# Kernel optimization log

Hardware: AMD Instinct MI355X
Metric: run time of the kernel (lower is better)

Reference implementation:

```python
import jax, jax.numpy as jnp
import numpy as np

N_NODES = 50000
N_EDGES = 800000
IN_CH, HID_CH, OUT_CH = 128, 128, 64


def setup_inputs() -> dict:
    key = jax.random.key(0)
    k1, k2, k3, k4, k5, k6 = jax.random.split(key, 6)
    x = jax.random.normal(k1, (N_NODES, IN_CH), dtype=jnp.float32)
    edge_index = jax.random.randint(k2, (2, N_EDGES), 0, N_NODES, dtype=jnp.int64)
    # nn.Linear params: W [out, in], b [out]
    W1 = jax.random.normal(k3, (HID_CH, IN_CH), dtype=jnp.float32) / np.sqrt(IN_CH)
    b1 = jax.random.normal(k4, (HID_CH,), dtype=jnp.float32) * 0.01
    W2 = jax.random.normal(k5, (OUT_CH, HID_CH), dtype=jnp.float32) / np.sqrt(HID_CH)
    b2 = jax.random.normal(k6, (OUT_CH,), dtype=jnp.float32) * 0.01
    return {"x": x, "edge_index": edge_index, "W1": W1, "b1": b1, "W2": W2, "b2": b2}


def _aggregate(x, edge_index):
    # Faithful to SimpleGNN.aggregate: deg from ROW counts, normalization gathered at DST (col).
    row, col = edge_index[0], edge_index[1]
    n = x.shape[0]
    deg = jnp.bincount(row, length=n).astype(x.dtype)
    deg_inv = jnp.where(deg > 0, 1.0 / deg, 0.0)
    # out[dst] += x[src] * deg_inv[dst]  ==  segment_sum(x[src] by dst) * deg_inv[dst]
    agg = jax.ops.segment_sum(x[row], col, num_segments=n)
    return agg * deg_inv[:, None]


def reference(x, edge_index, W1, b1, W2, b2):
    h = x @ W1.T + b1                 # [N, hidden]
    h = _aggregate(h, edge_index)     # degree-normalized scatter-add
    out = h @ W2.T + b2               # [N, out]
    return out
```

## Files before the change

kernel.cpp:

```cpp
#include <hip/hip_runtime.h>
#include <hip/hip_bf16.h>


#define IN_CH   128
#define OUT_CH  64
#define NCHUNK  64
#define NRANGE_H 4
#define RBINS_H 12544
#define MC_PAD  40
#define YROWS   32
#define PLACE_BLOCKS 256
#define SMEM_FLOATS (IN_CH * OUT_CH + YROWS * (IN_CH + 4))

typedef unsigned short u16;
typedef unsigned int u32;

static __device__ inline float bfu32_lo(u32 u) { return __uint_as_float(u << 16); }
static __device__ inline float bfu32_hi(u32 u) { return __uint_as_float(u & 0xffff0000u); }
static __device__ inline u16 f2bf(float f) {
    __hip_bfloat16 h = __float2bfloat16(f);
    return *reinterpret_cast<u16*>(&h);
}

static __device__ inline int detect_stride_wave(const int* __restrict__ ei) {
    int lane = threadIdx.x & 63;
    int idx = (lane < 32) ? (2 * lane + 1) : 1;
    int v = ei[idx];
    unsigned long long m = __ballot((v != 0) && (lane < 32));
    return (m == 0ull) ? 2 : 1;
}

static __device__ inline void y_unit(int t, const float* __restrict__ x,
                                     const float* __restrict__ M,
                                     u16* __restrict__ y, float* smem,
                                     int n_nodes) {
    int tid = threadIdx.x;
    float* Ms = smem;
    float (*xs)[IN_CH + 4] = (float(*)[IN_CH + 4])(smem + IN_CH * OUT_CH);
    int tx = tid & 15;
    int ty = tid >> 4;
    int row0 = t * YROWS;
    if (row0 >= n_nodes) return;

    const float4* Mv = (const float4*)M;
    float4* Msv = (float4*)Ms;
#pragma unroll
    for (int k = 0; k < 8; ++k) Msv[tid + 256 * k] = Mv[tid + 256 * k];

    for (int f = tid; f < YROWS * 32; f += 256) {
        int r = f >> 5, kq = f & 31;
        float4 v = make_float4(0.f, 0.f, 0.f, 0.f);
        if (row0 + r < n_nodes)
            v = *(const float4*)&x[(size_t)(row0 + r) * IN_CH + 4 * kq];
        *(float4*)&xs[r][4 * kq] = v;
    }
    __syncthreads();

    float4 acc0 = make_float4(0.f, 0.f, 0.f, 0.f);
    float4 acc1 = make_float4(0.f, 0.f, 0.f, 0.f);

    for (int k = 0; k < IN_CH; k += 4) {
        float4 xr0 = *(const float4*)&xs[ty][k];
        float4 xr1 = *(const float4*)&xs[ty + 16][k];
        float4 m0 = *(const float4*)&Ms[(k + 0) * OUT_CH + 4 * tx];
        float4 m1 = *(const float4*)&Ms[(k + 1) * OUT_CH + 4 * tx];
        float4 m2 = *(const float4*)&Ms[(k + 2) * OUT_CH + 4 * tx];
        float4 m3 = *(const float4*)&Ms[(k + 3) * OUT_CH + 4 * tx];
        acc0.x = fmaf(xr0.x, m0.x, acc0.x); acc0.y = fmaf(xr0.x, m0.y, acc0.y);
        acc0.z = fmaf(xr0.x, m0.z, acc0.z); acc0.w = fmaf(xr0.x, m0.w, acc0.w);
        acc0.x = fmaf(xr0.y, m1.x, acc0.x); acc0.y = fmaf(xr0.y, m1.y, acc0.y);
        acc0.z = fmaf(xr0.y, m1.z, acc0.z); acc0.w = fmaf(xr0.y, m1.w, acc0.w);
        acc0.x = fmaf(xr0.z, m2.x, acc0.x); acc0.y = fmaf(xr0.z, m2.y, acc0.y);
        acc0.z = fmaf(xr0.z, m2.z, acc0.z); acc0.w = fmaf(xr0.z, m2.w, acc0.w);
        acc0.x = fmaf(xr0.w, m3.x, acc0.x); acc0.y = fmaf(xr0.w, m3.y, acc0.y);
        acc0.z = fmaf(xr0.w, m3.z, acc0.z); acc0.w = fmaf(xr0.w, m3.w, acc0.w);
        acc1.x = fmaf(xr1.x, m0.x, acc1.x); acc1.y = fmaf(xr1.x, m0.y, acc1.y);
        acc1.z = fmaf(xr1.x, m0.z, acc1.z); acc1.w = fmaf(xr1.x, m0.w, acc1.w);
        acc1.x = fmaf(xr1.y, m1.x, acc1.x); acc1.y = fmaf(xr1.y, m1.y, acc1.y);
        acc1.z = fmaf(xr1.y, m1.z, acc1.z); acc1.w = fmaf(xr1.y, m1.w, acc1.w);
        acc1.x = fmaf(xr1.z, m2.x, acc1.x); acc1.y = fmaf(xr1.z, m2.y, acc1.y);
        acc1.z = fmaf(xr1.z, m2.z, acc1.z); acc1.w = fmaf(xr1.z, m2.w, acc1.w);
        acc1.x = fmaf(xr1.w, m3.x, acc1.x); acc1.y = fmaf(xr1.w, m3.y, acc1.y);
        acc1.z = fmaf(xr1.w, m3.z, acc1.z); acc1.w = fmaf(xr1.w, m3.w, acc1.w);
    }

    int r0 = row0 + ty;
    int r1 = row0 + ty + 16;
    if (r0 < n_nodes) {
        ushort4 s4;
        s4.x = f2bf(acc0.x); s4.y = f2bf(acc0.y);
        s4.z = f2bf(acc0.z); s4.w = f2bf(acc0.w);
        *(ushort4*)&y[(size_t)r0 * OUT_CH + 4 * tx] = s4;
    }
    if (r1 < n_nodes) {
        ushort4 s4;
        s4.x = f2bf(acc1.x); s4.y = f2bf(acc1.y);
        s4.z = f2bf(acc1.z); s4.w = f2bf(acc1.w);
        *(ushort4*)&y[(size_t)r1 * OUT_CH + 4 * tx] = s4;
    }
}

__global__ __launch_bounds__(256) void mk_prep(const float* __restrict__ W1,
                                               const float* __restrict__ b1,
                                               const float* __restrict__ W2,
                                               const int* __restrict__ ei,
                                               float* __restrict__ M,
                                               float* __restrict__ c,
                                               u16* __restrict__ row_slab,
                                               u16* __restrict__ col_slab,
                                               u16* __restrict__ erank,
                                               int* __restrict__ counter,
                                               int n_edges, int n_nodes) {
    __shared__ u32 bins[RBINS_H];
    int b = blockIdx.x;
    int tid = threadIdx.x;
    if (b < MC_PAD) {
        if (b == 0 && tid == 0) *counter = 0;
        int t = b * 256 + tid;
        if (t < IN_CH * OUT_CH) {
            int o = t & (OUT_CH - 1);
            int i = t >> 6;
            float acc = 0.f;
            for (int h = 0; h < 128; ++h)
                acc += W1[h * 128 + i] * W2[o * 128 + h];
            M[i * OUT_CH + o] = acc;
        } else if (t < IN_CH * OUT_CH + OUT_CH) {
            int o = t - IN_CH * OUT_CH;
            float acc = 0.f;
            for (int h = 0; h < 128; ++h)
                acc += b1[h] * W2[o * 128 + h];
            c[o] = acc;
        }
        return;
    }
    int hb = b - MC_PAD;
    int chunk = hb & (NCHUNK - 1);
    int range = hb >> 6;

    int range_size = (n_nodes + NRANGE_H - 1) / NRANGE_H;
    int lo = range * range_size;
    int hi = lo + range_size; if (hi > n_nodes) hi = n_nodes;
    int nbins = hi - lo;
    if (nbins <= 0) return;

    int stride = detect_stride_wave(ei);
    for (int i = tid; i < nbins; i += 256) bins[i] = 0u;
    __syncthreads();

    size_t e0 = (size_t)chunk * n_edges / NCHUNK;
    size_t e1 = (size_t)(chunk + 1) * n_edges / NCHUNK;
    size_t cnt = e1 - e0;
    const int* rp = ei;
    const int* cp = ei + (size_t)n_edges * stride;

    size_t i = tid;
    int s[8], d[8];
    for (; i + 1792 < cnt; i += 2048) {
#pragma unroll
        for (int k = 0; k < 8; ++k) s[k] = rp[(e0 + i + 256 * k) * stride];
#pragma unroll
        for (int k = 0; k < 8; ++k) d[k] = cp[(e0 + i + 256 * k) * stride];
#pragma unroll
        for (int k = 0; k < 8; ++k) {
            if (s[k] >= lo && s[k] < hi) atomicAdd(&bins[s[k] - lo], 1u);
            if (d[k] >= lo && d[k] < hi && (unsigned)s[k] < (unsigned)n_nodes) {
                u32 old = atomicAdd(&bins[d[k] - lo], 0x10000u);
                erank[e0 + i + 256 * k] = (u16)(old >> 16);
            }
        }
    }
    for (; i < cnt; i += 256) {
        int ss = rp[(e0 + i) * stride];
        int dd = cp[(e0 + i) * stride];
        if (ss >= lo && ss < hi) atomicAdd(&bins[ss - lo], 1u);
        if (dd >= lo && dd < hi && (unsigned)ss < (unsigned)n_nodes) {
            u32 old = atomicAdd(&bins[dd - lo], 0x10000u);
            erank[e0 + i] = (u16)(old >> 16);
        }
    }
    __syncthreads();

    size_t base = (size_t)chunk * n_nodes + lo;
    for (int k = tid; k < nbins; k += 256) {
        u32 v = bins[k];
        row_slab[base + k] = (u16)(v & 0xFFFFu);
        col_slab[base + k] = (u16)(v >> 16);
    }
}

__global__ __launch_bounds__(256) void mk_choff(u16* __restrict__ row_slab,
                                                u16* __restrict__ col_slab,
                                                int* __restrict__ deg_row,
                                                int* __restrict__ cnt_col,
                                                int* __restrict__ cursor_part,
                                                int* __restrict__ bsums,
                                                int* __restrict__ counter,
                                                int* __restrict__ bscan_g,
                                                int n_nodes, int nb) {
    __shared__ int sm[256];
    __shared__ int islast;
    int b = blockIdx.x;
    int t = threadIdx.x;
    int n = b * 256 + t;
    int run = 0;
    if (n < n_nodes) {
        int sum = 0;
#pragma unroll 8
        for (int ch = 0; ch < NCHUNK; ++ch)
            sum += row_slab[(size_t)ch * n_nodes + n];
        deg_row[n] = sum;
#pragma unroll 8
        for (int ch = 0; ch < NCHUNK; ++ch) {
            int v = col_slab[(size_t)ch * n_nodes + n];
            col_slab[(size_t)ch * n_nodes + n] = (u16)run;
            run += v;
        }
        cnt_col[n] = run;
    }
    sm[t] = run;
    __syncthreads();
    for (int d = 1; d < 256; d <<= 1) {
        int add = (t >= d) ? sm[t - d] : 0;
        __syncthreads();
        sm[t] += add;
        __syncthreads();
    }
    if (n < n_nodes) cursor_part[n] = sm[t] - run;
    if (t == 255) bsums[b] = sm[t];

    __syncthreads();
    if (t == 0) {
        __threadfence();
        int old = atomicAdd(counter, 1);
        islast = (old == nb - 1);
    }
    __syncthreads();
    if (islast) {
        int v = (t < nb) ? atomicAdd(&bsums[t], 0) : 0;
        sm[t] = v;
        __syncthreads();
        for (int d = 1; d < 256; d <<= 1) {
            int add = (t >= d) ? sm[t - d] : 0;
            __syncthreads();
            sm[t] += add;
            __syncthreads();
        }
        bscan_g[t] = sm[t] - v;
    }
}

__global__ __launch_bounds__(256) void mk_place_y(const int* __restrict__ ei,
                                                  const int* __restrict__ cursor_part,
                                                  const int* __restrict__ bscan_g,
                                                  const u16* __restrict__ col_slab,
                                                  const u16* __restrict__ erank,
                                                  int* __restrict__ csr_src,
                                                  const float* __restrict__ x,
                                                  const float* __restrict__ M,
                                                  u16* __restrict__ y,
                                                  int n_edges, int n_nodes) {
    __shared__ float smem[SMEM_FLOATS];
    int b = blockIdx.x;
    int tid = threadIdx.x;

    if (b < PLACE_BLOCKS) {
        int* bscanL = (int*)smem;
        bscanL[tid] = bscan_g[tid];
        __syncthreads();

        int chunk = b >> 2;
        int sub = b & 3;
        int stride = detect_stride_wave(ei);

        size_t e0 = (size_t)chunk * n_edges / NCHUNK;
        size_t e1 = (size_t)(chunk + 1) * n_edges / NCHUNK;
        size_t cnt = e1 - e0;
        size_t s0 = e0 + (size_t)sub * cnt / 4;
        size_t s1 = e0 + (size_t)(sub + 1) * cnt / 4;
        const int* rp = ei;
        const int* cp = ei + (size_t)n_edges * stride;
        size_t slab_base = (size_t)chunk * n_nodes;

        size_t i = s0 + tid;
        int s4[4], d4[4], cpart[4], coff[4];
        u16 r4[4];
        for (; i + 768 < s1; i += 1024) {
#pragma unroll
            for (int k = 0; k < 4; ++k) s4[k] = rp[(i + 256 * k) * stride];
#pragma unroll
            for (int k = 0; k < 4; ++k) d4[k] = cp[(i + 256 * k) * stride];
#pragma unroll
            for (int k = 0; k < 4; ++k) r4[k] = erank[i + 256 * k];
#pragma unroll
            for (int k = 0; k < 4; ++k) {
                int dc = ((unsigned)d4[k] < (unsigned)n_nodes) ? d4[k] : 0;
                cpart[k] = cursor_part[dc];
                coff[k]  = (int)col_slab[slab_base + dc];
            }
#pragma unroll
            for (int k = 0; k < 4; ++k) {
                if ((unsigned)d4[k] < (unsigned)n_nodes &&
                    (unsigned)s4[k] < (unsigned)n_nodes) {
                    csr_src[cpart[k] + bscanL[d4[k] >> 8] + coff[k] + (int)r4[k]] = s4[k];
                }
            }
        }
        for (; i < s1; i += 256) {
            int ss = rp[i * stride];
            int dd = cp[i * stride];
            if ((unsigned)dd < (unsigned)n_nodes && (unsigned)ss < (unsigned)n_nodes) {
                csr_src[cursor_part[dd] + bscanL[dd >> 8] +
                        (int)col_slab[slab_base + dd] + (int)erank[i]] = ss;
            }
        }
        return;
    }

    y_unit(b - PLACE_BLOCKS, x, M, y, smem, n_nodes);
}

__global__ __launch_bounds__(256) void mk_agg_final(const int* __restrict__ cursor_part,
                                                    const int* __restrict__ bscan_g,
                                                    const int* __restrict__ cnt_col,
                                                    const int* __restrict__ csr_src,
                                                    const int* __restrict__ deg_row,
                                                    const uint2* __restrict__ yv,
                                                    const float* __restrict__ c,
                                                    const float* __restrict__ b2,
                                                    float* __restrict__ out,
                                                    int n_nodes) {
    int wave = threadIdx.x >> 6;
    int lane = threadIdx.x & 63;
    int dsub = lane >> 4;
    int ch   = lane & 15;
    int d = blockIdx.x * 16 + wave * 4 + dsub;
    if (d >= n_nodes) return;

    int start = cursor_part[d] + bscan_g[d >> 8];
    int cnt = cnt_col[d];
    int end = start + cnt;
    int e1m = end - 1;
    float a0 = 0.f, a1 = 0.f, a2 = 0.f, a3 = 0.f;
    for (int j = start; j < end; j += 8) {
        int idx[8], srcs[8];
#pragma unroll
        for (int k = 0; k < 8; ++k) {
            int t = j + k;
            idx[k] = t > e1m ? e1m : t;
        }
#pragma unroll
        for (int k = 0; k < 8; ++k) srcs[k] = csr_src[idx[k]];
        uint2 u[8];
#pragma unroll
        for (int k = 0; k < 8; ++k) u[k] = yv[(size_t)srcs[k] * 16 + ch];
#pragma unroll
        for (int k = 1; k < 8; ++k)
            if (j + k >= end) { u[k].x = 0u; u[k].y = 0u; }
#pragma unroll
        for (int k = 0; k < 8; ++k) {
            a0 += bfu32_lo(u[k].x);
            a1 += bfu32_hi(u[k].x);
            a2 += bfu32_lo(u[k].y);
            a3 += bfu32_hi(u[k].y);
        }
    }
    int dr = deg_row[d];
    float di = (dr > 0) ? (1.0f / (float)dr) : 0.f;
    float fc = di * (float)cnt;
    float4 cv = ((const float4*)c)[ch];
    float4 bv = ((const float4*)b2)[ch];
    float4 o;
    o.x = di * a0 + fc * cv.x + bv.x;
    o.y = di * a1 + fc * cv.y + bv.y;
    o.z = di * a2 + fc * cv.z + bv.z;
    o.w = di * a3 + fc * cv.w + bv.w;
    ((float4*)(out + (size_t)d * OUT_CH))[ch] = o;
}

extern "C" void kernel_launch(void* const* d_in, const int* in_sizes, int n_in,
                              void* d_out, int out_size, void* d_ws, size_t ws_size,
                              hipStream_t stream) {
    const float* x  = (const float*)d_in[0];
    const int*   ei = (const int*)d_in[1];
    const float* W1 = (const float*)d_in[2];
    const float* b1 = (const float*)d_in[3];
    const float* W2 = (const float*)d_in[4];
    const float* b2 = (const float*)d_in[5];
    float* out = (float*)d_out;

    const int n_nodes = in_sizes[0] / IN_CH;
    const int n_edges = in_sizes[1] / 2;

    const size_t slab_bytes = (((size_t)NCHUNK * n_nodes * 2) + 127) & ~(size_t)127;
    const size_t csr_bytes  = ((size_t)n_edges * 4 + 127) & ~(size_t)127;
    const size_t y_bytes    = ((size_t)n_nodes * OUT_CH * 2 + 127) & ~(size_t)127;

    char* ws = (char*)d_ws;
    float* M        = (float*)(ws);
    float* c        = (float*)(ws + 32768);
    int*   deg_row  = (int*)  (ws + 33152);
    int*   cnt_col  = (int*)  (ws + 233216);
    int*   cursor   = (int*)  (ws + 433280);
    int*   bsums    = (int*)  (ws + 633344);
    int*   bscan_g  = (int*)  (ws + 634368);
    int*   counter  = (int*)  (ws + 635392);
    u16*   row_slab = (u16*)  (ws + 635520);
    u16*   col_slab = (u16*)  (ws + 635520 + slab_bytes);
    int*   csr_src  = (int*)  (ws + 635520 + 2 * slab_bytes);
    u16*   y        = (u16*)  (ws + 635520 + 2 * slab_bytes + csr_bytes);
    u16*   erank    = (u16*)  (ws + 635520 + 2 * slab_bytes + csr_bytes + y_bytes);

    const int y_total = (n_nodes + YROWS - 1) / YROWS;
    const int nb = (n_nodes + 255) / 256;

    mk_prep<<<MC_PAD + NCHUNK * NRANGE_H, 256, 0, stream>>>(
        W1, b1, W2, ei, M, c, row_slab, col_slab, erank, counter,
        n_edges, n_nodes);

    mk_choff<<<nb, 256, 0, stream>>>(row_slab, col_slab, deg_row, cnt_col,
                                     cursor, bsums, counter, bscan_g,
                                     n_nodes, nb);

    mk_place_y<<<PLACE_BLOCKS + y_total, 256, 0, stream>>>(
        ei, cursor, bscan_g, col_slab, erank, csr_src, x, M, y,
        n_edges, n_nodes);

    mk_agg_final<<<(n_nodes + 15) / 16, 256, 0, stream>>>(
        cursor, bscan_g, cnt_col, csr_src, deg_row, (const uint2*)y, c, b2, out,
        n_nodes);
}
```

Before: 158.4 us.

## Replace chunked shared-memory histogram slabs with global atomics for CSR build

Drops the per-chunk LDS histograms, u16 slab arrays and per-edge rank array used to build the destination-sorted CSR. Degree and column counts now come from global atomicAdd directly, and placement uses atomic cursor increments on the exclusive scan. This removes the slab write/read traffic and the 64-chunk reduction pass, and adds a zeroing kernel. The cost is heavy global atomic contention and a nondeterministic edge order within each destination. The aggregation start offset is recomputed from the post-increment cursor.

New measurement: 222.2 us. 40.3% more time.

```diff
diff --git a/kernel.cpp b/kernel.cpp
--- a/kernel.cpp
+++ b/kernel.cpp
@@ -4,12 +4,9 @@
 
 #define IN_CH   128
 #define OUT_CH  64
-#define NCHUNK  64
-#define NRANGE_H 4
-#define RBINS_H 12544
-#define MC_PAD  40
+#define MC_UNITS 33
 #define YROWS   32
-#define PLACE_BLOCKS 256
+#define EPB     2048
 #define SMEM_FLOATS (IN_CH * OUT_CH + YROWS * (IN_CH + 4))
 
 typedef unsigned short u16;
@@ -100,22 +97,25 @@
     }
 }
 
+__global__ __launch_bounds__(256) void mk_zero(float4* __restrict__ p, int n4,
+                                               int* __restrict__ counter) {
+    int i = blockIdx.x * 256 + threadIdx.x;
+    if (i < n4) p[i] = make_float4(0.f, 0.f, 0.f, 0.f);
+    if (i == 0) *counter = 0;
+}
+
 __global__ __launch_bounds__(256) void mk_prep(const float* __restrict__ W1,
                                                const float* __restrict__ b1,
                                                const float* __restrict__ W2,
                                                const int* __restrict__ ei,
                                                float* __restrict__ M,
                                                float* __restrict__ c,
-                                               u16* __restrict__ row_slab,
-                                               u16* __restrict__ col_slab,
-                                               u16* __restrict__ erank,
-                                               int* __restrict__ counter,
+                                               int* __restrict__ deg_row,
+                                               int* __restrict__ cnt_col,
                                                int n_edges, int n_nodes) {
-    __shared__ u32 bins[RBINS_H];
     int b = blockIdx.x;
     int tid = threadIdx.x;
-    if (b < MC_PAD) {
-        if (b == 0 && tid == 0) *counter = 0;
+    if (b < MC_UNITS) {
         int t = b * 256 + tid;
         if (t < IN_CH * OUT_CH) {
             int o = t & (OUT_CH - 1);
@@ -133,90 +133,53 @@
         }
         return;
     }
-    int hb = b - MC_PAD;
-    int chunk = hb & (NCHUNK - 1);
-    int range = hb >> 6;
-
-    int range_size = (n_nodes + NRANGE_H - 1) / NRANGE_H;
-    int lo = range * range_size;
-    int hi = lo + range_size; if (hi > n_nodes) hi = n_nodes;
-    int nbins = hi - lo;
-    if (nbins <= 0) return;
-
+    int db = b - MC_UNITS;
+    size_t e0 = (size_t)db * EPB;
+    if (e0 >= (size_t)n_edges) return;
     int stride = detect_stride_wave(ei);
-    for (int i = tid; i < nbins; i += 256) bins[i] = 0u;
-    __syncthreads();
-
-    size_t e0 = (size_t)chunk * n_edges / NCHUNK;
-    size_t e1 = (size_t)(chunk + 1) * n_edges / NCHUNK;
-    size_t cnt = e1 - e0;
     const int* rp = ei;
     const int* cp = ei + (size_t)n_edges * stride;
 
-    size_t i = tid;
-    int s[8], d[8];
-    for (; i + 1792 < cnt; i += 2048) {
-#pragma unroll
-        for (int k = 0; k < 8; ++k) s[k] = rp[(e0 + i + 256 * k) * stride];
-#pragma unroll
-        for (int k = 0; k < 8; ++k) d[k] = cp[(e0 + i + 256 * k) * stride];
+    size_t i0 = e0 + (size_t)tid * 8;
+    if (i0 + 8 <= (size_t)n_edges) {
+        int s8[8], d8[8];
+#pragma unroll
+        for (int k = 0; k < 8; ++k) s8[k] = rp[(i0 + k) * stride];
+#pragma unroll
+        for (int k = 0; k < 8; ++k) d8[k] = cp[(i0 + k) * stride];
 #pragma unroll
         for (int k = 0; k < 8; ++k) {
-            if (s[k] >= lo && s[k] < hi) atomicAdd(&bins[s[k] - lo], 1u);
-            if (d[k] >= lo && d[k] < hi && (unsigned)s[k] < (unsigned)n_nodes) {
-                u32 old = atomicAdd(&bins[d[k] - lo], 0x10000u);
-                erank[e0 + i + 256 * k] = (u16)(old >> 16);
-            }
-        }
-    }
-    for (; i < cnt; i += 256) {
-        int ss = rp[(e0 + i) * stride];
-        int dd = cp[(e0 + i) * stride];
-        if (ss >= lo && ss < hi) atomicAdd(&bins[ss - lo], 1u);
-        if (dd >= lo && dd < hi && (unsigned)ss < (unsigned)n_nodes) {
-            u32 old = atomicAdd(&bins[dd - lo], 0x10000u);
-            erank[e0 + i] = (u16)(old >> 16);
-        }
-    }
-    __syncthreads();
-
-    size_t base = (size_t)chunk * n_nodes + lo;
-    for (int k = tid; k < nbins; k += 256) {
-        u32 v = bins[k];
-        row_slab[base + k] = (u16)(v & 0xFFFFu);
-        col_slab[base + k] = (u16)(v >> 16);
-    }
-}
-
-__global__ __launch_bounds__(256) void mk_choff(u16* __restrict__ row_slab,
-                                                u16* __restrict__ col_slab,
-                                                int* __restrict__ deg_row,
-                                                int* __restrict__ cnt_col,
-                                                int* __restrict__ cursor_part,
-                                                int* __restrict__ bsums,
-                                                int* __restrict__ counter,
-                                                int* __restrict__ bscan_g,
-                                                int n_nodes, int nb) {
+            if ((unsigned)s8[k] < (unsigned)n_nodes) {
+                atomicAdd(&deg_row[s8[k]], 1);
+                if ((unsigned)d8[k] < (unsigned)n_nodes)
+                    atomicAdd(&cnt_col[d8[k]], 1);
+            }
+        }
+    } else {
+        for (size_t i = i0; i < (size_t)n_edges && i < i0 + 8; ++i) {
+            int ss = rp[i * stride];
+            int dd = cp[i * stride];
+            if ((unsigned)ss < (unsigned)n_nodes) {
+                atomicAdd(&deg_row[ss], 1);
+                if ((unsigned)dd < (unsigned)n_nodes)
+                    atomicAdd(&cnt_col[dd], 1);
+            }
+        }
+    }
+}
+
+__global__ __launch_bounds__(256) void mk_scan(const int* __restrict__ cnt_col,
+                                               int* __restrict__ cursor_part,
+                                               int* __restrict__ bsums,
+                                               int* __restrict__ counter,
+                                               int* __restrict__ bscan_g,
+                                               int n_nodes, int nb) {
     __shared__ int sm[256];
     __shared__ int islast;
     int b = blockIdx.x;
     int t = threadIdx.x;
     int n = b * 256 + t;
-    int run = 0;
-    if (n < n_nodes) {
-        int sum = 0;
-#pragma unroll 8
-        for (int ch = 0; ch < NCHUNK; ++ch)
-            sum += row_slab[(size_t)ch * n_nodes + n];
-        deg_row[n] = sum;
-#pragma unroll 8
-        for (int ch = 0; ch < NCHUNK; ++ch) {
-            int v = col_slab[(size_t)ch * n_nodes + n];
-            col_slab[(size_t)ch * n_nodes + n] = (u16)run;
-            run += v;
-        }
-        cnt_col[n] = run;
-    }
+    int run = (n < n_nodes) ? cnt_col[n] : 0;
     sm[t] = run;
     __syncthreads();
     for (int d = 1; d < 256; d <<= 1) {
@@ -250,73 +213,62 @@
 }
 
 __global__ __launch_bounds__(256) void mk_place_y(const int* __restrict__ ei,
-                                                  const int* __restrict__ cursor_part,
+                                                  int* __restrict__ cursor_part,
                                                   const int* __restrict__ bscan_g,
-                                                  const u16* __restrict__ col_slab,
-                                                  const u16* __restrict__ erank,
                                                   int* __restrict__ csr_src,
                                                   const float* __restrict__ x,
                                                   const float* __restrict__ M,
                                                   u16* __restrict__ y,
-                                                  int n_edges, int n_nodes) {
+                                                  int n_edges, int n_nodes,
+                                                  int place_blocks) {
     __shared__ float smem[SMEM_FLOATS];
     int b = blockIdx.x;
     int tid = threadIdx.x;
 
-    if (b < PLACE_BLOCKS) {
+    if (b < place_blocks) {
         int* bscanL = (int*)smem;
         bscanL[tid] = bscan_g[tid];
         __syncthreads();
 
-        int chunk = b >> 2;
-        int sub = b & 3;
+        size_t e0 = (size_t)b * EPB;
+        if (e0 >= (size_t)n_edges) return;
         int stride = detect_stride_wave(ei);
-
-        size_t e0 = (size_t)chunk * n_edges / NCHUNK;
-        size_t e1 = (size_t)(chunk + 1) * n_edges / NCHUNK;
-        size_t cnt = e1 - e0;
-        size_t s0 = e0 + (size_t)sub * cnt / 4;
-        size_t s1 = e0 + (size_t)(sub + 1) * cnt / 4;
         const int* rp = ei;
         const int* cp = ei + (size_t)n_edges * stride;
-        size_t slab_base = (size_t)chunk * n_nodes;
-
-        size_t i = s0 + tid;
-        int s4[4], d4[4], cpart[4], coff[4];
-        u16 r4[4];
-        for (; i + 768 < s1; i += 1024) {
-#pragma unroll
-            for (int k = 0; k < 4; ++k) s4[k] = rp[(i + 256 * k) * stride];
-#pragma unroll
-            for (int k = 0; k < 4; ++k) d4[k] = cp[(i + 256 * k) * stride];
-#pragma unroll
-            for (int k = 0; k < 4; ++k) r4[k] = erank[i + 256 * k];
-#pragma unroll
-            for (int k = 0; k < 4; ++k) {
-                int dc = ((unsigned)d4[k] < (unsigned)n_nodes) ? d4[k] : 0;
-                cpart[k] = cursor_part[dc];
-                coff[k]  = (int)col_slab[slab_base + dc];
-            }
-#pragma unroll
-            for (int k = 0; k < 4; ++k) {
-                if ((unsigned)d4[k] < (unsigned)n_nodes &&
-                    (unsigned)s4[k] < (unsigned)n_nodes) {
-                    csr_src[cpart[k] + bscanL[d4[k] >> 8] + coff[k] + (int)r4[k]] = s4[k];
+
+        size_t i0 = e0 + (size_t)tid * 8;
+        if (i0 + 8 <= (size_t)n_edges) {
+            int s8[8], d8[8], pos[8];
+#pragma unroll
+            for (int k = 0; k < 8; ++k) s8[k] = rp[(i0 + k) * stride];
+#pragma unroll
+            for (int k = 0; k < 8; ++k) d8[k] = cp[(i0 + k) * stride];
+#pragma unroll
+            for (int k = 0; k < 8; ++k) {
+                bool v = (unsigned)d8[k] < (unsigned)n_nodes &&
+                         (unsigned)s8[k] < (unsigned)n_nodes;
+                pos[k] = v ? atomicAdd(&cursor_part[d8[k]], 1) : -1;
+            }
+#pragma unroll
+            for (int k = 0; k < 8; ++k) {
+                if (pos[k] >= 0)
+                    csr_src[pos[k] + bscanL[d8[k] >> 8]] = s8[k];
+            }
+        } else {
+            for (size_t i = i0; i < (size_t)n_edges && i < i0 + 8; ++i) {
+                int ss = rp[i * stride];
+                int dd = cp[i * stride];
+                if ((unsigned)dd < (unsigned)n_nodes &&
+                    (unsigned)ss < (unsigned)n_nodes) {
+                    int p = atomicAdd(&cursor_part[dd], 1);
+                    csr_src[p + bscanL[dd >> 8]] = ss;
                 }
             }
         }
-        for (; i < s1; i += 256) {
-            int ss = rp[i * stride];
-            int dd = cp[i * stride];
-            if ((unsigned)dd < (unsigned)n_nodes && (unsigned)ss < (unsigned)n_nodes) {
-                csr_src[cursor_part[dd] + bscanL[dd >> 8] +
-                        (int)col_slab[slab_base + dd] + (int)erank[i]] = ss;
-            }
-        }
         return;
     }
 
-    y_unit(b - PLACE_BLOCKS, x, M, y, smem, n_nodes);
+    y_unit(b - place_blocks, x, M, y, smem, n_nodes);
 }
 
 __global__ __launch_bounds__(256) void mk_agg_final(const int* __restrict__ cursor_part,
@@ -336,8 +288,8 @@
     int d = blockIdx.x * 16 + wave * 4 + dsub;
     if (d >= n_nodes) return;
 
-    int start = cursor_part[d] + bscan_g[d >> 8];
     int cnt = cnt_col[d];
+    int start = cursor_part[d] - cnt + bscan_g[d >> 8];
     int end = start + cnt;
     int e1m = end - 1;
     float a0 = 0.f, a1 = 0.f, a2 = 0.f, a3 = 0.f;
@@ -391,9 +343,7 @@
     const int n_nodes = in_sizes[0] / IN_CH;
     const int n_edges = in_sizes[1] / 2;
 
-    const size_t slab_bytes = (((size_t)NCHUNK * n_nodes * 2) + 127) & ~(size_t)127;
-    const size_t csr_bytes  = ((size_t)n_edges * 4 + 127) & ~(size_t)127;
-    const size_t y_bytes    = ((size_t)n_nodes * OUT_CH * 2 + 127) & ~(size_t)127;
+    const size_t csr_bytes = ((size_t)n_edges * 4 + 127) & ~(size_t)127;
 
     char* ws = (char*)d_ws;
     float* M        = (float*)(ws);
@@ -404,26 +354,25 @@
     int*   bsums    = (int*)  (ws + 633344);
     int*   bscan_g  = (int*)  (ws + 634368);
     int*   counter  = (int*)  (ws + 635392);
-    u16*   row_slab = (u16*)  (ws + 635520);
-    u16*   col_slab = (u16*)  (ws + 635520 + slab_bytes);
-    int*   csr_src  = (int*)  (ws + 635520 + 2 * slab_bytes);
-    u16*   y        = (u16*)  (ws + 635520 + 2 * slab_bytes + csr_bytes);
-    u16*   erank    = (u16*)  (ws + 635520 + 2 * slab_bytes + csr_bytes + y_bytes);
+    int*   csr_src  = (int*)  (ws + 635520);
+    u16*   y        = (u16*)  (ws + 635520 + csr_bytes);
 
     const int y_total = (n_nodes + YROWS - 1) / YROWS;
     const int nb = (n_nodes + 255) / 256;
-
-    mk_prep<<<MC_PAD + NCHUNK * NRANGE_H, 256, 0, stream>>>(
-        W1, b1, W2, ei, M, c, row_slab, col_slab, erank, counter,
-        n_edges, n_nodes);
-
-    mk_choff<<<nb, 256, 0, stream>>>(row_slab, col_slab, deg_row, cnt_col,
-                                     cursor, bsums, counter, bscan_g,
-                                     n_nodes, nb);
-
-    mk_place_y<<<PLACE_BLOCKS + y_total, 256, 0, stream>>>(
-        ei, cursor, bscan_g, col_slab, erank, csr_src, x, M, y,
-        n_edges, n_nodes);
+    const int deg_blocks = (n_edges + EPB - 1) / EPB;
+    const int zero_n4 = (2 * 200064) / 16;
+
+    mk_zero<<<(zero_n4 + 255) / 256, 256, 0, stream>>>(
+        (float4*)deg_row, zero_n4, counter);
+
+    mk_prep<<<MC_UNITS + deg_blocks, 256, 0, stream>>>(
+        W1, b1, W2, ei, M, c, deg_row, cnt_col, n_edges, n_nodes);
+
+    mk_scan<<<nb, 256, 0, stream>>>(cnt_col, cursor, bsums, counter, bscan_g,
+                                    n_nodes, nb);
+
+    mk_place_y<<<deg_blocks + y_total, 256, 0, stream>>>(
+        ei, cursor, bscan_g, csr_src, x, M, y, n_edges, n_nodes, deg_blocks);
 
     mk_agg_final<<<(n_nodes + 15) / 16, 256, 0, stream>>>(
         cursor, bscan_g, cnt_col, csr_src, deg_row, (const uint2*)y, c, b2, out,
```
